# Kernel tuning notes

Measured on AMD Instinct MI355X. Metric: run time of the kernel, lower is better.

## Reference

```python
import jax, jax.numpy as jnp
import numpy as np

N = 100000      # nodes
E = 1200000     # edges (avg degree ~12)
D_IN = 64
D_OUT = 64


def setup_inputs() -> dict:
    key = jax.random.key(0)
    k1, k2, k3, k4 = jax.random.split(key, 4)
    x = jax.random.normal(k1, (N, D_IN), dtype=jnp.float32)
    # learned params (glorot-ish init)
    W = jax.random.normal(k2, (D_IN, D_OUT), dtype=jnp.float32) / np.sqrt(D_IN).astype(np.float32)
    b = jnp.zeros((D_OUT,), dtype=jnp.float32)
    src = jax.random.randint(k3, (E,), 0, N, dtype=jnp.int32)
    dst = jax.random.randint(k4, (E,), 0, N, dtype=jnp.int32)
    return {"x": x, "W": W, "b": b, "src": src, "dst": dst}


def reference(x, W, b, src, dst):
    # GCN layer: h = relu( D^-1/2 A D^-1/2 (x @ W) + b ), dropout=0 (eval)
    ones = jnp.ones(src.shape[0], dtype=x.dtype)
    deg_out = jax.ops.segment_sum(ones, src, num_segments=N)   # out-degree of source nodes
    deg_in = jax.ops.segment_sum(ones, dst, num_segments=N)    # in-degree of dest nodes
    norm_src = jax.lax.rsqrt(jnp.maximum(deg_out, 1.0))
    norm_dst = jax.lax.rsqrt(jnp.maximum(deg_in, 1.0))

    h = x @ W                                                  # [N, D_OUT] dense transform
    msg = h[src] * norm_src[src][:, None]                      # [E, D_OUT] gathered, pre-normalized messages
    agg = jax.ops.segment_sum(msg, dst, num_segments=N)        # [N, D_OUT] sparse aggregation
    out = agg * norm_dst[:, None] + b
    return jax.nn.relu(out)
```

## Files before the change

### kernel.cpp

```cpp
#include <hip/hip_runtime.h>
#include <hip/hip_bf16.h>

#define N_NODES 100000
#define N_EDGES 1200000
#define NPAIRS  (N_EDGES / 2)
#define DCH 64

typedef __attribute__((ext_vector_type(8))) short bf16x8;
typedef __attribute__((ext_vector_type(4))) float f32x4;

#define K1B 256
#define K1T 1024
#define NRID 2
#define RID_NODES 50000
#define RID_WORDS 12500
#define HSLICE_PAIRS 4688
#define SCAT_PAIRS ((NPAIRS + K1B - 1) / K1B)

#define BNODES 128
#define KBUK ((N_NODES + BNODES - 1) / BNODES)
#define CAPE 3008
#define CAPN 40

#define NTILES (N_NODES / 16)
#define GWAVES (K1B * K1T / 64)

#define K3T 512

#define OFF_DEG      0
#define OFF_GCUR     100096
#define OFF_FLAG     103296
#define OFF_ESORT    103424
#define OFF_HS       9512704

__device__ __forceinline__ float load_f(const void* p, int i, int f32) {
    if (f32) return ((const float*)p)[i];
    return __bfloat162float(((const __hip_bfloat16*)p)[i]);
}

__device__ __forceinline__ unsigned short f2bf_bits(float f) {
    __hip_bfloat16 h = __float2bfloat16(f);
    return __builtin_bit_cast(unsigned short, h);
}

__global__ __launch_bounds__(K1T, 4)
void fused_kernel(const int* __restrict__ src,
                  const int* __restrict__ dst,
                  const void* __restrict__ x,
                  const void* __restrict__ W,
                  unsigned int* __restrict__ deg_packed,
                  int* __restrict__ gcur,
                  unsigned int* __restrict__ esort,
                  int* __restrict__ flag,
                  __hip_bfloat16* __restrict__ hs) {
    __shared__ __align__(16) char smem[RID_WORDS * 4];
    __shared__ int sn;
    int tid = threadIdx.x, bid = blockIdx.x;

    if (tid == 0) sn = 0;
    __syncthreads();
    if (tid < 256) {
        const unsigned short* u = (const unsigned short*)x;
        int c = 0;
        for (int i = tid * 16; i < tid * 16 + 16; ++i) {
            unsigned short v = u[2 * i];
            int e = (v >> 7) & 0xFF;
            if (e >= 141) c++;
        }
        if (c) atomicAdd(&sn, c);
    }
    __syncthreads();
    int f32 = sn > 256;
    if (bid == 0 && tid == 0) *flag = f32;

    {
        float* wt = (float*)smem;
        for (int i = tid; i < DCH * DCH; i += K1T)
            wt[i] = load_f(W, i, f32);
        __syncthreads();

        int lane = tid & 63;
        int cB = lane & 15;
        int k0 = (lane >> 4) * 8;

        bf16x8 bf00, bf01, bf10, bf11, bf20, bf21, bf30, bf31;
#define LDB(DST, CT, KH) { bf16x8 t;                                      \
    _Pragma("unroll")                                                     \
    for (int j = 0; j < 8; ++j)                                           \
        t[j] = (short)f2bf_bits(wt[((KH)*32 + k0 + j) * DCH + (CT)*16 + cB]); \
    DST = t; }
        LDB(bf00, 0, 0) LDB(bf01, 0, 1)
        LDB(bf10, 1, 0) LDB(bf11, 1, 1)
        LDB(bf20, 2, 0) LDB(bf21, 2, 1)
        LDB(bf30, 3, 0) LDB(bf31, 3, 1)
#undef LDB

        int wid = bid * (K1T / 64) + (tid >> 6);
        int rowA = lane & 15;
        for (int t = wid; t < NTILES; t += GWAVES) {
            int nbase = t << 4;
            int node = nbase + rowA;
            bf16x8 a0, a1;
            if (f32) {
                const float* xr = (const float*)x + node * DCH + k0;
                float4 p0 = *(const float4*)(xr);
                float4 p1 = *(const float4*)(xr + 4);
                float4 p2 = *(const float4*)(xr + 32);
                float4 p3 = *(const float4*)(xr + 36);
                a0[0] = (short)f2bf_bits(p0.x); a0[1] = (short)f2bf_bits(p0.y);
                a0[2] = (short)f2bf_bits(p0.z); a0[3] = (short)f2bf_bits(p0.w);
                a0[4] = (short)f2bf_bits(p1.x); a0[5] = (short)f2bf_bits(p1.y);
                a0[6] = (short)f2bf_bits(p1.z); a0[7] = (short)f2bf_bits(p1.w);
                a1[0] = (short)f2bf_bits(p2.x); a1[1] = (short)f2bf_bits(p2.y);
                a1[2] = (short)f2bf_bits(p2.z); a1[3] = (short)f2bf_bits(p2.w);
                a1[4] = (short)f2bf_bits(p3.x); a1[5] = (short)f2bf_bits(p3.y);
                a1[6] = (short)f2bf_bits(p3.z); a1[7] = (short)f2bf_bits(p3.w);
            } else {
                const short* xr = (const short*)x + node * DCH + k0;
                a0 = *(const bf16x8*)(xr);
                a1 = *(const bf16x8*)(xr + 32);
            }
            f32x4 ac0 = {0.f,0.f,0.f,0.f}, ac1 = {0.f,0.f,0.f,0.f};
            f32x4 ac2 = {0.f,0.f,0.f,0.f}, ac3 = {0.f,0.f,0.f,0.f};
            ac0 = __builtin_amdgcn_mfma_f32_16x16x32_bf16(a0, bf00, ac0, 0, 0, 0);
            ac1 = __builtin_amdgcn_mfma_f32_16x16x32_bf16(a0, bf10, ac1, 0, 0, 0);
            ac2 = __builtin_amdgcn_mfma_f32_16x16x32_bf16(a0, bf20, ac2, 0, 0, 0);
            ac3 = __builtin_amdgcn_mfma_f32_16x16x32_bf16(a0, bf30, ac3, 0, 0, 0);
            ac0 = __builtin_amdgcn_mfma_f32_16x16x32_bf16(a1, bf01, ac0, 0, 0, 0);
            ac1 = __builtin_amdgcn_mfma_f32_16x16x32_bf16(a1, bf11, ac1, 0, 0, 0);
            ac2 = __builtin_amdgcn_mfma_f32_16x16x32_bf16(a1, bf21, ac2, 0, 0, 0);
            ac3 = __builtin_amdgcn_mfma_f32_16x16x32_bf16(a1, bf31, ac3, 0, 0, 0);

            int rbase = nbase + (lane >> 4) * 4;
#pragma unroll
            for (int r = 0; r < 4; ++r) {
                int n = rbase + r;
                __hip_bfloat16* ho = hs + n * DCH + cB;
                ho[0]  = __float2bfloat16(ac0[r]);
                ho[16] = __float2bfloat16(ac1[r]);
                ho[32] = __float2bfloat16(ac2[r]);
                ho[48] = __float2bfloat16(ac3[r]);
            }
        }
    }
    __syncthreads();

    {
        unsigned int* h = (unsigned int*)smem;
        int rid = bid & (NRID - 1);
        int j   = bid >> 1;
        for (int w = tid; w < RID_WORDS; w += K1T) h[w] = 0;
        __syncthreads();
        int lo = rid * RID_NODES;
        const int2* s2 = (const int2*)src;
        int p0 = j * HSLICE_PAIRS;
        int p1 = p0 + HSLICE_PAIRS; if (p1 > NPAIRS) p1 = NPAIRS;
        for (int p = p0 + tid; p < p1; p += K1T) {
            int2 sp = s2[p];
            int n0 = sp.x - lo, n1 = sp.y - lo;
            if ((unsigned)n0 < (unsigned)RID_NODES)
                atomicAdd(&h[n0 >> 2], 1u << ((n0 & 3) * 8));
            if ((unsigned)n1 < (unsigned)RID_NODES)
                atomicAdd(&h[n1 >> 2], 1u << ((n1 & 3) * 8));
        }
        __syncthreads();
        unsigned int* dp = deg_packed + rid * RID_WORDS;
        for (int w = tid; w < RID_WORDS; w += K1T) {
            unsigned int v = h[w];
            if (v) atomicAdd(&dp[w], v);
        }
        __syncthreads();
    }

    {
        int2* ssrc = (int2*)smem;
        int2* sdst = (int2*)(smem + SCAT_PAIRS * 8);
        int*  cnt  = (int*)(smem + SCAT_PAIRS * 16);
        int*  base = cnt + KBUK;
        int*  cur  = base + KBUK;
        int p0 = bid * SCAT_PAIRS;
        int p1 = p0 + SCAT_PAIRS; if (p1 > NPAIRS) p1 = NPAIRS;
        int npair = p1 - p0;
        const int2* s2 = (const int2*)(src + 2 * p0);
        const int2* d2 = (const int2*)(dst + 2 * p0);
        for (int i = tid; i < KBUK; i += K1T) { cnt[i] = 0; cur[i] = 0; }
        __syncthreads();
        for (int p = tid; p < npair; p += K1T) {
            int2 sp = s2[p];
            int2 dp = d2[p];
            ssrc[p] = sp;
            sdst[p] = dp;
            atomicAdd(&cnt[dp.x >> 7], 1);
            atomicAdd(&cnt[dp.y >> 7], 1);
        }
        __syncthreads();
        for (int i = tid; i < KBUK; i += K1T)
            if (cnt[i]) base[i] = atomicAdd(&gcur[i], cnt[i]);
        __syncthreads();
        for (int p = tid; p < npair; p += K1T) {
            int2 sp = ssrc[p];
            int2 dp = sdst[p];
            int b0 = dp.x >> 7, b1 = dp.y >> 7;
            int pos0 = base[b0] + atomicAdd(&cur[b0], 1);
            if (pos0 < CAPE)
                esort[b0 * CAPE + pos0] =
                    (unsigned int)sp.x | ((unsigned int)(dp.x & 127) << 24);
            int pos1 = base[b1] + atomicAdd(&cur[b1], 1);
            if (pos1 < CAPE)
                esort[b1 * CAPE + pos1] =
                    (unsigned int)sp.y | ((unsigned int)(dp.y & 127) << 24);
        }
    }
}

__global__ __launch_bounds__(K3T, 6)
void gather_kernel(const __hip_bfloat16* __restrict__ hs,
                   const unsigned int* __restrict__ esort,
                   const int* __restrict__ gcur,
                   const unsigned int* __restrict__ deg_packed,
                   const void* __restrict__ b,
                   const int* __restrict__ flag,
                   void* __restrict__ out) {
    __shared__ unsigned int slots[BNODES * CAPN];
    __shared__ int cur[BNODES];
    __shared__ float tab[256];
    int k = blockIdx.x, tid = threadIdx.x;
    int bbase = k * CAPE;
    int m = gcur[k];
    if (m > CAPE) m = CAPE;

    if (tid < BNODES) cur[tid] = 0;
    if (tid < 256) tab[tid] = rsqrtf(fmaxf((float)tid, 1.0f));
    __syncthreads();
    for (int e = tid; e < m; e += K3T) {
        unsigned int w = esort[bbase + e];
        int r = w >> 24;
        unsigned int s = w & 0xFFFFFFu;
        unsigned int dw = deg_packed[s >> 2];
        unsigned int degb = (dw >> ((s & 3) * 8)) & 0xFFu;
        int pos = atomicAdd(&cur[r], 1);
        if (pos < CAPN) slots[r * CAPN + pos] = s | (degb << 24);
    }
    __syncthreads();

    int f32 = *flag;
    int lane = tid & 63, wv = tid >> 6;
    int q = lane >> 4;
    int cg = lane & 15;
    const unsigned short* hsu = (const unsigned short*)hs;
    float b0 = load_f(b, cg * 4 + 0, f32);
    float b1 = load_f(b, cg * 4 + 1, f32);
    float b2 = load_f(b, cg * 4 + 2, f32);
    float b3 = load_f(b, cg * 4 + 3, f32);
    int nlo = k * BNODES;

#define ACC(ACCV, U, F) \
    (ACCV).x = fmaf(__uint_as_float((U).x << 16),         (F), (ACCV).x); \
    (ACCV).y = fmaf(__uint_as_float((U).x & 0xFFFF0000u), (F), (ACCV).y); \
    (ACCV).z = fmaf(__uint_as_float((U).y << 16),         (F), (ACCV).z); \
    (ACCV).w = fmaf(__uint_as_float((U).y & 0xFFFF0000u), (F), (ACCV).w);

    for (int base = wv; base < BNODES; base += 16) {
        int tA = base, tB = base + 8;
        int degA = cur[tA], degB = cur[tB];
        int dA = degA < CAPN ? degA : CAPN;
        int dB = degB < CAPN ? degB : CAPN;
        const unsigned int* eA = slots + tA * CAPN;
        const unsigned int* eB = slots + tB * CAPN;
        float4 aA0 = {0.f,0.f,0.f,0.f}, aA1 = {0.f,0.f,0.f,0.f};
        float4 aA2 = {0.f,0.f,0.f,0.f}, aA3 = {0.f,0.f,0.f,0.f};
        float4 aB0 = {0.f,0.f,0.f,0.f}, aB1 = {0.f,0.f,0.f,0.f};
        float4 aB2 = {0.f,0.f,0.f,0.f}, aB3 = {0.f,0.f,0.f,0.f};
        int dmax = dA > dB ? dA : dB;
        for (int j0 = 0; j0 < dmax; j0 += 16) {
            int i0 = j0 + q, i1 = j0 + 4 + q, i2 = j0 + 8 + q, i3 = j0 + 12 + q;
            unsigned int wA0 = (i0 < dA) ? eA[i0] : 0u;
            unsigned int wA1 = (i1 < dA) ? eA[i1] : 0u;
            unsigned int wA2 = (i2 < dA) ? eA[i2] : 0u;
            unsigned int wA3 = (i3 < dA) ? eA[i3] : 0u;
            unsigned int wB0 = (i0 < dB) ? eB[i0] : 0u;
            unsigned int wB1 = (i1 < dB) ? eB[i1] : 0u;
            unsigned int wB2 = (i2 < dB) ? eB[i2] : 0u;
            unsigned int wB3 = (i3 < dB) ? eB[i3] : 0u;
            uint2 uA0 = ((const uint2*)(hsu + (wA0 & 0xFFFFFFu) * DCH))[cg];
            uint2 uA1 = ((const uint2*)(hsu + (wA1 & 0xFFFFFFu) * DCH))[cg];
            uint2 uA2 = ((const uint2*)(hsu + (wA2 & 0xFFFFFFu) * DCH))[cg];
            uint2 uA3 = ((const uint2*)(hsu + (wA3 & 0xFFFFFFu) * DCH))[cg];
            uint2 uB0 = ((const uint2*)(hsu + (wB0 & 0xFFFFFFu) * DCH))[cg];
            uint2 uB1 = ((const uint2*)(hsu + (wB1 & 0xFFFFFFu) * DCH))[cg];
            uint2 uB2 = ((const uint2*)(hsu + (wB2 & 0xFFFFFFu) * DCH))[cg];
            uint2 uB3 = ((const uint2*)(hsu + (wB3 & 0xFFFFFFu) * DCH))[cg];
            float fA0 = tab[wA0 >> 24], fA1 = tab[wA1 >> 24];
            float fA2 = tab[wA2 >> 24], fA3 = tab[wA3 >> 24];
            float fB0 = tab[wB0 >> 24], fB1 = tab[wB1 >> 24];
            float fB2 = tab[wB2 >> 24], fB3 = tab[wB3 >> 24];
            if (i0 < dA) { ACC(aA0, uA0, fA0) }
            if (i1 < dA) { ACC(aA1, uA1, fA1) }
            if (i2 < dA) { ACC(aA2, uA2, fA2) }
            if (i3 < dA) { ACC(aA3, uA3, fA3) }
            if (i0 < dB) { ACC(aB0, uB0, fB0) }
            if (i1 < dB) { ACC(aB1, uB1, fB1) }
            if (i2 < dB) { ACC(aB2, uB2, fB2) }
            if (i3 < dB) { ACC(aB3, uB3, fB3) }
        }
        float4 oA, oB;
        oA.x = (aA0.x + aA1.x) + (aA2.x + aA3.x);
        oA.y = (aA0.y + aA1.y) + (aA2.y + aA3.y);
        oA.z = (aA0.z + aA1.z) + (aA2.z + aA3.z);
        oA.w = (aA0.w + aA1.w) + (aA2.w + aA3.w);
        oB.x = (aB0.x + aB1.x) + (aB2.x + aB3.x);
        oB.y = (aB0.y + aB1.y) + (aB2.y + aB3.y);
        oB.z = (aB0.z + aB1.z) + (aB2.z + aB3.z);
        oB.w = (aB0.w + aB1.w) + (aB2.w + aB3.w);
        oA.x += __shfl_xor(oA.x, 16); oA.y += __shfl_xor(oA.y, 16);
        oA.z += __shfl_xor(oA.z, 16); oA.w += __shfl_xor(oA.w, 16);
        oA.x += __shfl_xor(oA.x, 32); oA.y += __shfl_xor(oA.y, 32);
        oA.z += __shfl_xor(oA.z, 32); oA.w += __shfl_xor(oA.w, 32);
        oB.x += __shfl_xor(oB.x, 16); oB.y += __shfl_xor(oB.y, 16);
        oB.z += __shfl_xor(oB.z, 16); oB.w += __shfl_xor(oB.w, 16);
        oB.x += __shfl_xor(oB.x, 32); oB.y += __shfl_xor(oB.y, 32);
        oB.z += __shfl_xor(oB.z, 32); oB.w += __shfl_xor(oB.w, 32);
        int myNode = nlo + ((lane < 16) ? tA : tB);
        int myDeg  = (lane < 16) ? degA : degB;
        float4 o   = (lane < 16) ? oA : oB;
        if (lane < 32 && myNode < N_NODES) {
            float nrm = rsqrtf(fmaxf((float)myDeg, 1.0f));
            o.x = fmaxf(o.x * nrm + b0, 0.0f);
            o.y = fmaxf(o.y * nrm + b1, 0.0f);
            o.z = fmaxf(o.z * nrm + b2, 0.0f);
            o.w = fmaxf(o.w * nrm + b3, 0.0f);
            if (f32) {
                ((float4*)out)[myNode * 16 + cg] = o;
            } else {
                ushort4 s;
                s.x = f2bf_bits(o.x);
                s.y = f2bf_bits(o.y);
                s.z = f2bf_bits(o.z);
                s.w = f2bf_bits(o.w);
                ((ushort4*)out)[myNode * 16 + cg] = s;
            }
        }
    }
#undef ACC
}

extern "C" void kernel_launch(void* const* d_in, const int* in_sizes, int n_in,
                              void* d_out, int out_size, void* d_ws, size_t ws_size,
                              hipStream_t stream) {
    const void* x   = d_in[0];
    const void* W   = d_in[1];
    const void* b   = d_in[2];
    const int*  src = (const int*)d_in[3];
    const int*  dst = (const int*)d_in[4];

    char* ws = (char*)d_ws;
    unsigned int* deg_packed = (unsigned int*)(ws + OFF_DEG);
    int* gcur     = (int*)(ws + OFF_GCUR);
    int* flag     = (int*)(ws + OFF_FLAG);
    unsigned int* esort = (unsigned int*)(ws + OFF_ESORT);
    __hip_bfloat16* hs  = (__hip_bfloat16*)(ws + OFF_HS);

    (void)hipMemsetAsync(ws, 0, OFF_FLAG + 4, stream);

    fused_kernel<<<K1B, K1T, 0, stream>>>(
        src, dst, x, W, deg_packed, gcur, esort, flag, hs);

    gather_kernel<<<KBUK, K3T, 0, stream>>>(
        hs, esort, gcur, deg_packed, b, flag, d_out);
}
```

Baseline: 156.7 us.

## Make gather kernel persistent and deepen per-iteration gather unrolling

```diff
diff --git a/kernel.cpp b/kernel.cpp
--- a/kernel.cpp
+++ b/kernel.cpp
@@ -26,6 +26,7 @@
 #define GWAVES (K1B * K1T / 64)
 
 #define K3T 512
+#define K3B 768
 
 #define OFF_DEG      0
 #define OFF_GCUR     100096
@@ -224,25 +225,7 @@
     __shared__ unsigned int slots[BNODES * CAPN];
     __shared__ int cur[BNODES];
     __shared__ float tab[256];
-    int k = blockIdx.x, tid = threadIdx.x;
-    int bbase = k * CAPE;
-    int m = gcur[k];
-    if (m > CAPE) m = CAPE;
-
-    if (tid < BNODES) cur[tid] = 0;
-    if (tid < 256) tab[tid] = rsqrtf(fmaxf((float)tid, 1.0f));
-    __syncthreads();
-    for (int e = tid; e < m; e += K3T) {
-        unsigned int w = esort[bbase + e];
-        int r = w >> 24;
-        unsigned int s = w & 0xFFFFFFu;
-        unsigned int dw = deg_packed[s >> 2];
-        unsigned int degb = (dw >> ((s & 3) * 8)) & 0xFFu;
-        int pos = atomicAdd(&cur[r], 1);
-        if (pos < CAPN) slots[r * CAPN + pos] = s | (degb << 24);
-    }
-    __syncthreads();
-
+    int tid = threadIdx.x;
     int f32 = *flag;
     int lane = tid & 63, wv = tid >> 6;
     int q = lane >> 4;
@@ -252,7 +235,8 @@
     float b1 = load_f(b, cg * 4 + 1, f32);
     float b2 = load_f(b, cg * 4 + 2, f32);
     float b3 = load_f(b, cg * 4 + 3, f32);
-    int nlo = k * BNODES;
+    if (tid < 256)
+        tab[tid] = (tid == 255) ? 0.0f : rsqrtf(fmaxf((float)tid, 1.0f));
 
 #define ACC(ACCV, U, F) \
     (ACCV).x = fmaf(__uint_as_float((U).x << 16),         (F), (ACCV).x); \
@@ -260,86 +244,109 @@
     (ACCV).z = fmaf(__uint_as_float((U).y << 16),         (F), (ACCV).z); \
     (ACCV).w = fmaf(__uint_as_float((U).y & 0xFFFF0000u), (F), (ACCV).w);
 
-    for (int base = wv; base < BNODES; base += 16) {
-        int tA = base, tB = base + 8;
-        int degA = cur[tA], degB = cur[tB];
-        int dA = degA < CAPN ? degA : CAPN;
-        int dB = degB < CAPN ? degB : CAPN;
-        const unsigned int* eA = slots + tA * CAPN;
-        const unsigned int* eB = slots + tB * CAPN;
-        float4 aA0 = {0.f,0.f,0.f,0.f}, aA1 = {0.f,0.f,0.f,0.f};
-        float4 aA2 = {0.f,0.f,0.f,0.f}, aA3 = {0.f,0.f,0.f,0.f};
-        float4 aB0 = {0.f,0.f,0.f,0.f}, aB1 = {0.f,0.f,0.f,0.f};
-        float4 aB2 = {0.f,0.f,0.f,0.f}, aB3 = {0.f,0.f,0.f,0.f};
-        int dmax = dA > dB ? dA : dB;
-        for (int j0 = 0; j0 < dmax; j0 += 16) {
-            int i0 = j0 + q, i1 = j0 + 4 + q, i2 = j0 + 8 + q, i3 = j0 + 12 + q;
-            unsigned int wA0 = (i0 < dA) ? eA[i0] : 0u;
-            unsigned int wA1 = (i1 < dA) ? eA[i1] : 0u;
-            unsigned int wA2 = (i2 < dA) ? eA[i2] : 0u;
-            unsigned int wA3 = (i3 < dA) ? eA[i3] : 0u;
-            unsigned int wB0 = (i0 < dB) ? eB[i0] : 0u;
-            unsigned int wB1 = (i1 < dB) ? eB[i1] : 0u;
-            unsigned int wB2 = (i2 < dB) ? eB[i2] : 0u;
-            unsigned int wB3 = (i3 < dB) ? eB[i3] : 0u;
-            uint2 uA0 = ((const uint2*)(hsu + (wA0 & 0xFFFFFFu) * DCH))[cg];
-            uint2 uA1 = ((const uint2*)(hsu + (wA1 & 0xFFFFFFu) * DCH))[cg];
-            uint2 uA2 = ((const uint2*)(hsu + (wA2 & 0xFFFFFFu) * DCH))[cg];
-            uint2 uA3 = ((const uint2*)(hsu + (wA3 & 0xFFFFFFu) * DCH))[cg];
-            uint2 uB0 = ((const uint2*)(hsu + (wB0 & 0xFFFFFFu) * DCH))[cg];
-            uint2 uB1 = ((const uint2*)(hsu + (wB1 & 0xFFFFFFu) * DCH))[cg];
-            uint2 uB2 = ((const uint2*)(hsu + (wB2 & 0xFFFFFFu) * DCH))[cg];
-            uint2 uB3 = ((const uint2*)(hsu + (wB3 & 0xFFFFFFu) * DCH))[cg];
-            float fA0 = tab[wA0 >> 24], fA1 = tab[wA1 >> 24];
-            float fA2 = tab[wA2 >> 24], fA3 = tab[wA3 >> 24];
-            float fB0 = tab[wB0 >> 24], fB1 = tab[wB1 >> 24];
-            float fB2 = tab[wB2 >> 24], fB3 = tab[wB3 >> 24];
-            if (i0 < dA) { ACC(aA0, uA0, fA0) }
-            if (i1 < dA) { ACC(aA1, uA1, fA1) }
-            if (i2 < dA) { ACC(aA2, uA2, fA2) }
-            if (i3 < dA) { ACC(aA3, uA3, fA3) }
-            if (i0 < dB) { ACC(aB0, uB0, fB0) }
-            if (i1 < dB) { ACC(aB1, uB1, fB1) }
-            if (i2 < dB) { ACC(aB2, uB2, fB2) }
-            if (i3 < dB) { ACC(aB3, uB3, fB3) }
-        }
-        float4 oA, oB;
-        oA.x = (aA0.x + aA1.x) + (aA2.x + aA3.x);
-        oA.y = (aA0.y + aA1.y) + (aA2.y + aA3.y);
-        oA.z = (aA0.z + aA1.z) + (aA2.z + aA3.z);
-        oA.w = (aA0.w + aA1.w) + (aA2.w + aA3.w);
-        oB.x = (aB0.x + aB1.x) + (aB2.x + aB3.x);
-        oB.y = (aB0.y + aB1.y) + (aB2.y + aB3.y);
-        oB.z = (aB0.z + aB1.z) + (aB2.z + aB3.z);
-        oB.w = (aB0.w + aB1.w) + (aB2.w + aB3.w);
-        oA.x += __shfl_xor(oA.x, 16); oA.y += __shfl_xor(oA.y, 16);
-        oA.z += __shfl_xor(oA.z, 16); oA.w += __shfl_xor(oA.w, 16);
-        oA.x += __shfl_xor(oA.x, 32); oA.y += __shfl_xor(oA.y, 32);
-        oA.z += __shfl_xor(oA.z, 32); oA.w += __shfl_xor(oA.w, 32);
-        oB.x += __shfl_xor(oB.x, 16); oB.y += __shfl_xor(oB.y, 16);
-        oB.z += __shfl_xor(oB.z, 16); oB.w += __shfl_xor(oB.w, 16);
-        oB.x += __shfl_xor(oB.x, 32); oB.y += __shfl_xor(oB.y, 32);
-        oB.z += __shfl_xor(oB.z, 32); oB.w += __shfl_xor(oB.w, 32);
-        int myNode = nlo + ((lane < 16) ? tA : tB);
-        int myDeg  = (lane < 16) ? degA : degB;
-        float4 o   = (lane < 16) ? oA : oB;
-        if (lane < 32 && myNode < N_NODES) {
-            float nrm = rsqrtf(fmaxf((float)myDeg, 1.0f));
-            o.x = fmaxf(o.x * nrm + b0, 0.0f);
-            o.y = fmaxf(o.y * nrm + b1, 0.0f);
-            o.z = fmaxf(o.z * nrm + b2, 0.0f);
-            o.w = fmaxf(o.w * nrm + b3, 0.0f);
-            if (f32) {
-                ((float4*)out)[myNode * 16 + cg] = o;
-            } else {
-                ushort4 s;
-                s.x = f2bf_bits(o.x);
-                s.y = f2bf_bits(o.y);
-                s.z = f2bf_bits(o.z);
-                s.w = f2bf_bits(o.w);
-                ((ushort4*)out)[myNode * 16 + cg] = s;
+    for (int k = blockIdx.x; k < KBUK; k += K3B) {
+        if (tid < BNODES) cur[tid] = 0;
+        __syncthreads();
+        int bbase = k * CAPE;
+        int m = gcur[k];
+        if (m > CAPE) m = CAPE;
+        for (int e = tid; e < m; e += K3T) {
+            unsigned int w = esort[bbase + e];
+            int r = w >> 24;
+            unsigned int s = w & 0xFFFFFFu;
+            unsigned int dw = deg_packed[s >> 2];
+            unsigned int degb = (dw >> ((s & 3) * 8)) & 0xFFu;
+            int pos = atomicAdd(&cur[r], 1);
+            if (pos < CAPN) slots[r * CAPN + pos] = s | (degb << 24);
+        }
+        __syncthreads();
+
+        int nlo = k * BNODES;
+        for (int base = wv; base < BNODES; base += 16) {
+            int tA = base, tB = base + 8;
+            int degA = cur[tA], degB = cur[tB];
+            int dA = degA < CAPN ? degA : CAPN;
+            int dB = degB < CAPN ? degB : CAPN;
+            const unsigned int* eA = slots + tA * CAPN;
+            const unsigned int* eB = slots + tB * CAPN;
+            float4 aA0 = {0.f,0.f,0.f,0.f}, aA1 = {0.f,0.f,0.f,0.f};
+            float4 aA2 = {0.f,0.f,0.f,0.f}, aA3 = {0.f,0.f,0.f,0.f};
+            float4 aB0 = {0.f,0.f,0.f,0.f}, aB1 = {0.f,0.f,0.f,0.f};
+            float4 aB2 = {0.f,0.f,0.f,0.f}, aB3 = {0.f,0.f,0.f,0.f};
+            int dmax = dA > dB ? dA : dB;
+            for (int j0 = 0; j0 < dmax; j0 += 32) {
+                unsigned int wA[8], wB[8];
+#pragma unroll
+                for (int p = 0; p < 8; ++p) {
+                    int i = j0 + p * 4 + q;
+                    wA[p] = (i < dA) ? eA[i] : 0xFF000000u;
+                    wB[p] = (i < dB) ? eB[i] : 0xFF000000u;
+                }
+                uint2 uA[8], uB[8];
+#pragma unroll
+                for (int p = 0; p < 8; ++p) {
+                    uA[p] = ((const uint2*)(hsu + (wA[p] & 0xFFFFFFu) * DCH))[cg];
+                    uB[p] = ((const uint2*)(hsu + (wB[p] & 0xFFFFFFu) * DCH))[cg];
+                }
+                {
+                    float f;
+                    f = tab[wA[0] >> 24]; ACC(aA0, uA[0], f)
+                    f = tab[wA[1] >> 24]; ACC(aA1, uA[1], f)
+                    f = tab[wA[2] >> 24]; ACC(aA2, uA[2], f)
+                    f = tab[wA[3] >> 24]; ACC(aA3, uA[3], f)
+                    f = tab[wA[4] >> 24]; ACC(aA0, uA[4], f)
+                    f = tab[wA[5] >> 24]; ACC(aA1, uA[5], f)
+                    f = tab[wA[6] >> 24]; ACC(aA2, uA[6], f)
+                    f = tab[wA[7] >> 24]; ACC(aA3, uA[7], f)
+                    f = tab[wB[0] >> 24]; ACC(aB0, uB[0], f)
+                    f = tab[wB[1] >> 24]; ACC(aB1, uB[1], f)
+                    f = tab[wB[2] >> 24]; ACC(aB2, uB[2], f)
+                    f = tab[wB[3] >> 24]; ACC(aB3, uB[3], f)
+                    f = tab[wB[4] >> 24]; ACC(aB0, uB[4], f)
+                    f = tab[wB[5] >> 24]; ACC(aB1, uB[5], f)
+                    f = tab[wB[6] >> 24]; ACC(aB2, uB[6], f)
+                    f = tab[wB[7] >> 24]; ACC(aB3, uB[7], f)
+                }
             }
-        }
+            float4 oA, oB;
+            oA.x = (aA0.x + aA1.x) + (aA2.x + aA3.x);
+            oA.y = (aA0.y + aA1.y) + (aA2.y + aA3.y);
+            oA.z = (aA0.z + aA1.z) + (aA2.z + aA3.z);
+            oA.w = (aA0.w + aA1.w) + (aA2.w + aA3.w);
+            oB.x = (aB0.x + aB1.x) + (aB2.x + aB3.x);
+            oB.y = (aB0.y + aB1.y) + (aB2.y + aB3.y);
+            oB.z = (aB0.z + aB1.z) + (aB2.z + aB3.z);
+            oB.w = (aB0.w + aB1.w) + (aB2.w + aB3.w);
+            oA.x += __shfl_xor(oA.x, 16); oA.y += __shfl_xor(oA.y, 16);
+            oA.z += __shfl_xor(oA.z, 16); oA.w += __shfl_xor(oA.w, 16);
+            oA.x += __shfl_xor(oA.x, 32); oA.y += __shfl_xor(oA.y, 32);
+            oA.z += __shfl_xor(oA.z, 32); oA.w += __shfl_xor(oA.w, 32);
+            oB.x += __shfl_xor(oB.x, 16); oB.y += __shfl_xor(oB.y, 16);
+            oB.z += __shfl_xor(oB.z, 16); oB.w += __shfl_xor(oB.w, 16);
+            oB.x += __shfl_xor(oB.x, 32); oB.y += __shfl_xor(oB.y, 32);
+            oB.z += __shfl_xor(oB.z, 32); oB.w += __shfl_xor(oB.w, 32);
+            int myNode = nlo + ((lane < 16) ? tA : tB);
+            int myDeg  = (lane < 16) ? degA : degB;
+            float4 o   = (lane < 16) ? oA : oB;
+            if (lane < 32 && myNode < N_NODES) {
+                float nrm = rsqrtf(fmaxf((float)myDeg, 1.0f));
+                o.x = fmaxf(o.x * nrm + b0, 0.0f);
+                o.y = fmaxf(o.y * nrm + b1, 0.0f);
+                o.z = fmaxf(o.z * nrm + b2, 0.0f);
+                o.w = fmaxf(o.w * nrm + b3, 0.0f);
+                if (f32) {
+                    ((float4*)out)[myNode * 16 + cg] = o;
+                } else {
+                    ushort4 s;
+                    s.x = f2bf_bits(o.x);
+                    s.y = f2bf_bits(o.y);
+                    s.z = f2bf_bits(o.z);
+                    s.w = f2bf_bits(o.w);
+                    ((ushort4*)out)[myNode * 16 + cg] = s;
+                }
+            }
+        }
+        __syncthreads();
     }
 #undef ACC
 }
@@ -365,6 +372,6 @@
     fused_kernel<<<K1B, K1T, 0, stream>>>(
         src, dst, x, W, deg_packed, gcur, esort, flag, hs);
 
-    gather_kernel<<<KBUK, K3T, 0, stream>>>(
+    gather_kernel<<<K3B, K3T, 0, stream>>>(
         hs, esort, gcur, deg_packed, b, flag, d_out);
 }
```

After: 199.8 us. +27.5%, slower.
